# Performance work log

Measured on AMD Instinct MI355X. Metric: run time of the kernel, lower is better.

## Reference

```python
import jax, jax.numpy as jnp
from jax import lax
import numpy as np

RADIUS = 0.1
NSAMPLE = 32
STRIDE = 4
NUM_DIR = 32
BN_EPS = 1e-5


def _fps(p, m):
    # furthest point sampling: p (B,N,3) -> (B,m) int32 indices, start at index 0
    B, N, _ = p.shape

    def step(carry, _):
        dists, last = carry
        lp = jnp.take_along_axis(p, jnp.broadcast_to(last[:, None, None], (B, 1, 3)), axis=1)
        d = jnp.sum((p - lp) ** 2, axis=-1)
        dists = jnp.minimum(dists, d)
        nxt = jnp.argmax(dists, axis=-1).astype(jnp.int32)
        return (dists, nxt), nxt

    last0 = jnp.zeros((B,), jnp.int32)
    d0 = jnp.full((B, N), 1e10, p.dtype)
    _, rest = lax.scan(step, (d0, last0), None, length=m - 1)
    return jnp.concatenate([last0[None, :], rest], axis=0).T  # (B, m)


def _ball_query(q, p, k, radius):
    # q (B,M,3) centers, p (B,N,3) support -> (B,M,k) indices of first k points in ball,
    # padded with the first found index (PointNet++ convention)
    N = p.shape[1]
    d2 = jnp.sum((q[:, :, None, :] - p[:, None, :, :]) ** 2, axis=-1)  # (B,M,N)
    cand = jnp.where(d2 < radius * radius, jnp.arange(N, dtype=jnp.int32), N)
    cand = jnp.sort(cand, axis=-1)[:, :, :k]
    first = cand[:, :, :1]
    return jnp.where(cand == N, first, cand)


def _bn(x, g, b, m, v):
    # BatchNorm1d eval mode on (B,C,N)
    return (x - m[:, None]) * (g[:, None] / jnp.sqrt(v[:, None] + BN_EPS)) + b[:, None]


def _normalize(x, axis):
    return x / jnp.maximum(jnp.linalg.norm(x, axis=axis, keepdims=True), 1e-12)


def setup_inputs() -> dict:
    key = jax.random.key(0)
    ks = jax.random.split(key, 16)
    B, N, Cin, Cout = 4, 8192, 128, 256
    half = Cout // 2
    s = 0.02
    return {
        "p": jax.random.uniform(ks[0], (B, N, 3), jnp.float32),
        "f": jax.random.normal(ks[1], (B, Cin, N), jnp.float32),
        "conv1_w": jax.random.normal(ks[2], (Cout, Cin), jnp.float32) * s,
        "conv1_b": jax.random.normal(ks[3], (Cout,), jnp.float32) * s,
        "skip_w": jax.random.normal(ks[4], (Cout, Cin), jnp.float32) * s,
        "skip_b": jax.random.normal(ks[5], (Cout,), jnp.float32) * s,
        "bn1_g": jnp.ones((Cout,), jnp.float32),
        "bn1_b": jnp.zeros((Cout,), jnp.float32),
        "bn1_m": jax.random.normal(ks[6], (Cout,), jnp.float32) * 0.1,
        "bn1_v": jax.random.uniform(ks[7], (Cout,), jnp.float32) + 0.5,
        "dir_vectors": jax.random.normal(ks[8], (NUM_DIR, 3), jnp.float32),
        "de_w1": jax.random.normal(ks[9], (half, NUM_DIR), jnp.float32) * s,
        "de_g": jnp.ones((half,), jnp.float32),
        "de_bb": jnp.zeros((half,), jnp.float32),
        "de_m": jax.random.normal(ks[10], (half,), jnp.float32) * 0.1,
        "de_v": jax.random.uniform(ks[11], (half,), jnp.float32) + 0.5,
        "de_w2": jax.random.normal(ks[12], (Cout, half), jnp.float32) * s,
        "de_b2": jax.random.normal(ks[13], (Cout,), jnp.float32) * s,
    }


def reference(p, f, conv1_w, conv1_b, skip_w, skip_b, bn1_g, bn1_b, bn1_m, bn1_v,
              dir_vectors, de_w1, de_g, de_bb, de_m, de_v, de_w2, de_b2):
    B, N, _ = p.shape
    Cout = conv1_w.shape[0]
    M, K = N // STRIDE, NSAMPLE

    # FPS sampling + centroid gather
    idx = _fps(p, M)  # (B,M)
    new_p = jnp.take_along_axis(p, jnp.broadcast_to(idx[:, :, None], (B, M, 3)), axis=1)

    # residual branch: gather input feats at centroids, 1x1 conv (bn_after=False)
    fi = jnp.take_along_axis(f, jnp.broadcast_to(idx[:, None, :], (B, f.shape[1], M)), axis=2)
    identity = jnp.einsum('oc,bcm->bom', skip_w, fi) + skip_b[:, None]

    # convs1: 1x1 conv on all N points
    f1 = jnp.einsum('oc,bcn->bon', conv1_w, f) + conv1_b[:, None]  # (B,Cout,N)

    # ball-query grouping
    qidx = _ball_query(new_p, p, K, RADIUS)  # (B,M,K)
    idxf = qidx.reshape(B, M * K)
    gp = jnp.take_along_axis(p, jnp.broadcast_to(idxf[:, :, None], (B, M * K, 3)), axis=1).reshape(B, M, K, 3)
    dp = jnp.transpose(gp - new_p[:, :, None, :], (0, 3, 1, 2))  # (B,3,M,K)
    fj = jnp.take_along_axis(f1, jnp.broadcast_to(idxf[:, None, :], (B, Cout, M * K)), axis=2).reshape(B, Cout, M, K)

    # directional encoding
    dpn = _normalize(dp, axis=1)
    vec = _normalize(dir_vectors, axis=1)  # (NUM_DIR,3)
    theta = jnp.einsum('md,bdnk->bmnk', vec, dpn)  # (B,NUM_DIR,M,K)
    tmax = theta.max(axis=-1)  # (B,NUM_DIR,M)
    h = jnp.einsum('om,bmn->bon', de_w1, tmax)
    h = jax.nn.gelu(_bn(h, de_g, de_bb, de_m, de_v), approximate=False)
    pe = jnp.einsum('oc,bcn->bon', de_w2, h) + de_b2[:, None]

    # neighbor max-pool + BN + residuals
    f_out = _bn(fj.max(axis=-1), bn1_g, bn1_b, bn1_m, bn1_v) + pe + identity
    return new_p, f_out
```

## Files before the change

### kernel.cpp

```cpp
#include <hip/hip_runtime.h>

#define BATCH 4
#define NPTS 8192
#define MPTS 2048
#define CIN 128
#define CO 256
#define KS 32
#define ND 32
#define HALF 128

typedef unsigned int u32;
typedef unsigned long long u64;

#define DPPC_QUAD_XOR1 0xB1
#define DPPC_QUAD_XOR2 0x4E
#define DPPC_ROW_MIRROR 0x140
#define DPPC_ROW_HALF_MIRROR 0x141
#define DPPC_ROW_BCAST15 0x142
#define DPPC_ROW_BCAST31 0x143

template<int CTRL>
__device__ __forceinline__ float dpp_max(float v) {
    int o = __builtin_amdgcn_update_dpp(__float_as_int(-1e30f), __float_as_int(v),
                                        CTRL, 0xF, 0xF, false);
    return fmaxf(v, __int_as_float(o));
}
__device__ __forceinline__ float wave_max_f32(float v) {
    v = dpp_max<DPPC_QUAD_XOR1>(v);
    v = dpp_max<DPPC_QUAD_XOR2>(v);
    v = dpp_max<DPPC_ROW_HALF_MIRROR>(v);
    v = dpp_max<DPPC_ROW_MIRROR>(v);
    v = dpp_max<DPPC_ROW_BCAST15>(v);
    v = dpp_max<DPPC_ROW_BCAST31>(v);
    return __int_as_float(__builtin_amdgcn_readlane(__float_as_int(v), 63));
}

__global__ __launch_bounds__(512) void k_fps(const float* __restrict__ p,
                                             float* __restrict__ out_newp,
                                             int* __restrict__ idx) {
    __shared__ u64 wkey[2][8];
    int b = blockIdx.x, t = threadIdx.x;
    int lane = t & 63, wid = t >> 6;
    const float* pb = p + (size_t)b * NPTS * 3;
    float x[16], y[16], z[16], dist[16];
    int j0 = t * 16;
#pragma unroll
    for (int i = 0; i < 16; ++i) {
        x[i] = pb[(j0 + i) * 3 + 0];
        y[i] = pb[(j0 + i) * 3 + 1];
        z[i] = pb[(j0 + i) * 3 + 2];
        dist[i] = 1e10f;
    }
    float lx = pb[0], ly = pb[1], lz = pb[2];
    if (t == 0) {
        out_newp[(size_t)b * MPTS * 3 + 0] = lx;
        out_newp[(size_t)b * MPTS * 3 + 1] = ly;
        out_newp[(size_t)b * MPTS * 3 + 2] = lz;
        idx[b * MPTS] = 0;
    }
    for (int s = 1; s < MPTS; ++s) {
        int par = s & 1;
        float bv = -1e30f; int bi = 0;
#pragma unroll
        for (int i = 0; i < 16; ++i) {
            float dx = __fsub_rn(x[i], lx);
            float dy = __fsub_rn(y[i], ly);
            float dz = __fsub_rn(z[i], lz);
            float d  = __fadd_rn(__fadd_rn(__fmul_rn(dx, dx), __fmul_rn(dy, dy)),
                                 __fmul_rn(dz, dz));
            float nd = fminf(dist[i], d);
            dist[i] = nd;
            bool gt = nd > bv;
            bi = gt ? i : bi;
            bv = fmaxf(bv, nd);
        }
        float gmw = wave_max_f32(bv);
        u64 mask = __ballot(bv == gmw);
        int first = __ffsll((long long)mask) - 1;
        if (lane == first) {
            int cand = j0 + bi;
            wkey[par][wid] = ((u64)__float_as_uint(gmw) << 32)
                           | (u64)(u32)(NPTS - 1 - cand);
        }
        __syncthreads();
        u64 bestk = wkey[par][0];
#pragma unroll
        for (int ww = 1; ww < 8; ++ww) {
            u64 kk = wkey[par][ww];
            if (kk > bestk) bestk = kk;
        }
        int w0 = (NPTS - 1 - (int)(bestk & 0xFFFFFFFFull)) & (NPTS - 1);
        lx = pb[w0 * 3 + 0]; ly = pb[w0 * 3 + 1]; lz = pb[w0 * 3 + 2];
        if (t == 0) {
            idx[b * MPTS + s] = w0;
            out_newp[((size_t)b * MPTS + s) * 3 + 0] = lx;
            out_newp[((size_t)b * MPTS + s) * 3 + 1] = ly;
            out_newp[((size_t)b * MPTS + s) * 3 + 2] = lz;
        }
    }
}

__global__ __launch_bounds__(256) void k_featz(
    const float* __restrict__ p, const float* __restrict__ f,
    const float* __restrict__ conv1_w, const float* __restrict__ conv1_b,
    const float* __restrict__ skip_w,  const float* __restrict__ skip_b,
    const float* __restrict__ bn1_g, const float* __restrict__ bn1_b,
    const float* __restrict__ bn1_m, const float* __restrict__ bn1_v,
    const float* __restrict__ dirv,  const float* __restrict__ de_w1,
    const float* __restrict__ de_g,  const float* __restrict__ de_bb,
    const float* __restrict__ de_m,  const float* __restrict__ de_v,
    const float* __restrict__ de_w2, const float* __restrict__ de_b2,
    const int* __restrict__ idx,     float* __restrict__ out_f) {
    __shared__ __align__(16) float fg[KS * CIN];
    __shared__ float sdx[KS], sdy[KS], sdz[KS];
    __shared__ float ltm[ND], lfi[CIN], lh[HALF];
    __shared__ int swidx[4][KS];
    __shared__ int scnt[4];
    __shared__ int nb[KS], nbp[KS];

    int q = blockIdx.x;
    int b = q >> 11;
    int m = q & (MPTS - 1);
    int t = threadIdx.x, lane = t & 63, w = t >> 6;
    const float* pb = p + (size_t)b * NPTS * 3;
    int i0 = idx[q] & (NPTS - 1);
    float qx = pb[i0 * 3 + 0], qy = pb[i0 * 3 + 1], qz = pb[i0 * 3 + 2];
    const float R2 = 0.1f * 0.1f;

    int cnt = 0;
    int seg = w * 2048;
    for (int base = 0; base < 2048; base += 64) {
        int j = seg + base + lane;
        float dx = __fsub_rn(pb[j * 3 + 0], qx);
        float dy = __fsub_rn(pb[j * 3 + 1], qy);
        float dz = __fsub_rn(pb[j * 3 + 2], qz);
        float d2 = __fadd_rn(__fadd_rn(__fmul_rn(dx, dx), __fmul_rn(dy, dy)),
                             __fmul_rn(dz, dz));
        bool hit = d2 < R2;
        u64 mask = __ballot(hit);
        if (hit) {
            int pos = cnt + __popcll(mask & ((1ull << lane) - 1ull));
            if (pos < KS) swidx[w][pos] = j;
        }
        cnt += __popcll(mask);
        if (cnt >= KS) break;
    }
    if (lane == 0) scnt[w] = cnt < KS ? cnt : KS;
    __syncthreads();
    int c0s = scnt[0], c1s = scnt[1], c2s = scnt[2], c3s = scnt[3];
    int st1 = c0s, st2 = c0s + c1s, st3 = c0s + c1s + c2s;
    int total = c0s + c1s + c2s + c3s; if (total > KS) total = KS;
    if (total < 1) total = 1;
    if (t < 128) {
        int ww = t >> 5, l = t & 31;
        int stw = (ww == 0) ? 0 : (ww == 1) ? st1 : (ww == 2) ? st2 : st3;
        int cw  = (ww == 0) ? c0s : (ww == 1) ? c1s : (ww == 2) ? c2s : c3s;
        int gp = stw + l;
        if (l < cw && gp < KS) nb[gp] = swidx[ww][l];
    }
    __syncthreads();
    if (t < KS) {
        int jk = nb[t < total ? t : 0] & (NPTS - 1);
        nbp[t] = jk;
        float dx = pb[jk * 3 + 0] - qx;
        float dy = pb[jk * 3 + 1] - qy;
        float dz = pb[jk * 3 + 2] - qz;
        float nr = fmaxf(sqrtf(dx * dx + dy * dy + dz * dz), 1e-12f);
        sdx[t] = dx / nr; sdy[t] = dy / nr; sdz[t] = dz / nr;
    }
    if (t >= 128) {
        lfi[t - 128] = f[((size_t)b * CIN + (t - 128)) * NPTS + i0];
    }
    __syncthreads();
    if (t < ND) {
        float ax = dirv[t * 3], ay = dirv[t * 3 + 1], az = dirv[t * 3 + 2];
        float n = fmaxf(sqrtf(ax * ax + ay * ay + az * az), 1e-12f);
        float vx = ax / n, vy = ay / n, vz = az / n;
        float tm = -1e30f;
#pragma unroll
        for (int k = 0; k < KS; ++k)
            tm = fmaxf(tm, vx * sdx[k] + vy * sdy[k] + vz * sdz[k]);
        ltm[t] = tm;
    }
    for (int e = t; e < KS * CIN; e += 256) {
        int k = e >> 7, i = e & 127;
        fg[k * CIN + i] = f[((size_t)b * CIN + i) * NPTS + nbp[k]];
    }
    __syncthreads();

    int c = t;
    float acc[KS];
#pragma unroll
    for (int k = 0; k < KS; ++k) acc[k] = 0.0f;
    const float4* w4 = (const float4*)(conv1_w + (size_t)c * CIN);
    const float4* fg4 = (const float4*)fg;
    for (int i4 = 0; i4 < 32; ++i4) {
        float4 wv = w4[i4];
#pragma unroll 8
        for (int k = 0; k < KS; ++k) {
            float4 g = fg4[k * 32 + i4];
            acc[k] = fmaf(wv.x, g.x, fmaf(wv.y, g.y,
                     fmaf(wv.z, g.z, fmaf(wv.w, g.w, acc[k]))));
        }
    }
    float bias = conv1_b[c];
    float mx = -1e30f;
#pragma unroll
    for (int k = 0; k < KS; ++k) mx = fmaxf(mx, acc[k] + bias);
    float sc1 = bn1_g[c] / sqrtf(bn1_v[c] + 1e-5f);
    float o1 = (mx - bn1_m[c]) * sc1 + bn1_b[c];

    float idv = skip_b[c];
    {
        const float4* sr = (const float4*)(skip_w + (size_t)c * CIN);
#pragma unroll 8
        for (int r = 0; r < 32; ++r) {
            float4 v = sr[r];
            idv = fmaf(v.x, lfi[r*4+0], fmaf(v.y, lfi[r*4+1],
                  fmaf(v.z, lfi[r*4+2], fmaf(v.w, lfi[r*4+3], idv))));
        }
    }

    {
        int hc = c & (HALF - 1);
        const float4* d1 = (const float4*)(de_w1 + (size_t)hc * ND);
        float a = 0.0f;
#pragma unroll
        for (int r = 0; r < 8; ++r) {
            float4 v = d1[r];
            a = fmaf(v.x, ltm[r*4+0], fmaf(v.y, ltm[r*4+1],
                fmaf(v.z, ltm[r*4+2], fmaf(v.w, ltm[r*4+3], a))));
        }
        float dsc = de_g[hc] / sqrtf(de_v[hc] + 1e-5f);
        float xb = (a - de_m[hc]) * dsc + de_bb[hc];
        float hv = 0.5f * xb * (1.0f + erff(xb * 0.70710678118654752440f));
        if (c < HALF) lh[c] = hv;
    }
    __syncthreads();
    float pe = de_b2[c];
    {
        const float4* d2p = (const float4*)(de_w2 + (size_t)c * HALF);
#pragma unroll 8
        for (int r = 0; r < 32; ++r) {
            float4 v = d2p[r];
            pe = fmaf(v.x, lh[r*4+0], fmaf(v.y, lh[r*4+1],
                 fmaf(v.z, lh[r*4+2], fmaf(v.w, lh[r*4+3], pe))));
        }
    }
    out_f[((size_t)b * CO + c) * MPTS + m] = o1 + pe + idv;
}

extern "C" void kernel_launch(void* const* d_in, const int* in_sizes, int n_in,
                              void* d_out, int out_size, void* d_ws, size_t ws_size,
                              hipStream_t stream) {
    const float* p       = (const float*)d_in[0];
    const float* f       = (const float*)d_in[1];
    const float* conv1_w = (const float*)d_in[2];
    const float* conv1_b = (const float*)d_in[3];
    const float* skip_w  = (const float*)d_in[4];
    const float* skip_b  = (const float*)d_in[5];
    const float* bn1_g   = (const float*)d_in[6];
    const float* bn1_b   = (const float*)d_in[7];
    const float* bn1_m   = (const float*)d_in[8];
    const float* bn1_v   = (const float*)d_in[9];
    const float* dirv    = (const float*)d_in[10];
    const float* de_w1   = (const float*)d_in[11];
    const float* de_g    = (const float*)d_in[12];
    const float* de_bb   = (const float*)d_in[13];
    const float* de_m    = (const float*)d_in[14];
    const float* de_v    = (const float*)d_in[15];
    const float* de_w2   = (const float*)d_in[16];
    const float* de_b2   = (const float*)d_in[17];

    float* out_newp = (float*)d_out;
    float* out_f    = (float*)d_out + (size_t)BATCH * MPTS * 3;
    int*   idx      = (int*)d_ws;

    k_fps  <<<dim3(BATCH),        dim3(512), 0, stream>>>(p, out_newp, idx);
    k_featz<<<dim3(BATCH * MPTS), dim3(256), 0, stream>>>(
        p, f, conv1_w, conv1_b, skip_w, skip_b, bn1_g, bn1_b, bn1_m, bn1_v,
        dirv, de_w1, de_g, de_bb, de_m, de_v, de_w2, de_b2, idx, out_f);
}
```

Measured before the change: 3.091 ms.

## Precompute conv1 over all points and simplify FPS winner lookup

The conv1 1x1 convolution moves out of the per-centroid kernel. A new kernel computes it once for all N points into a transposed workspace buffer, and the feature kernel gathers and max-pools neighbour rows from it instead of recomputing 32x128x256 FMAs per centroid. The FPS kernel now passes the winning point's coordinates through shared memory rather than reloading them from global memory, and stages outputs in LDS with a single write at the end. The new path needs a large workspace and falls back to a per-batch or fully fused path when the workspace is too small.

```diff
diff --git a/kernel.cpp b/kernel.cpp
--- a/kernel.cpp
+++ b/kernel.cpp
@@ -39,6 +39,9 @@
                                              float* __restrict__ out_newp,
                                              int* __restrict__ idx) {
     __shared__ u64 wkey[2][8];
+    __shared__ float wcx[2][8], wcy[2][8], wcz[2][8];
+    __shared__ float obuf[MPTS * 3];
+    __shared__ int   oidx[MPTS];
     int b = blockIdx.x, t = threadIdx.x;
     int lane = t & 63, wid = t >> 6;
     const float* pb = p + (size_t)b * NPTS * 3;
@@ -51,13 +54,12 @@
         z[i] = pb[(j0 + i) * 3 + 2];
         dist[i] = 1e10f;
     }
+#pragma unroll
+    for (int i = 0; i < 16; ++i) {
+        asm volatile("" : "+v"(x[i]), "+v"(y[i]), "+v"(z[i]));
+    }
     float lx = pb[0], ly = pb[1], lz = pb[2];
-    if (t == 0) {
-        out_newp[(size_t)b * MPTS * 3 + 0] = lx;
-        out_newp[(size_t)b * MPTS * 3 + 1] = ly;
-        out_newp[(size_t)b * MPTS * 3 + 2] = lz;
-        idx[b * MPTS] = 0;
-    }
+    if (t == 0) { obuf[0] = lx; obuf[1] = ly; obuf[2] = lz; oidx[0] = 0; }
     for (int s = 1; s < MPTS; ++s) {
         int par = s & 1;
         float bv = -1e30f; int bi = 0;
@@ -78,29 +80,213 @@
         u64 mask = __ballot(bv == gmw);
         int first = __ffsll((long long)mask) - 1;
         if (lane == first) {
-            int cand = j0 + bi;
+            float sx = x[0], sy = y[0], sz = z[0];
+#pragma unroll
+            for (int k = 1; k < 16; ++k) {
+                if (bi == k) { sx = x[k]; sy = y[k]; sz = z[k]; }
+            }
             wkey[par][wid] = ((u64)__float_as_uint(gmw) << 32)
-                           | (u64)(u32)(NPTS - 1 - cand);
+                           | (u64)(u32)(NPTS - 1 - (j0 + bi));
+            wcx[par][wid] = sx; wcy[par][wid] = sy; wcz[par][wid] = sz;
         }
         __syncthreads();
-        u64 bestk = wkey[par][0];
+        u64 bestk = wkey[par][0]; int bw = 0;
 #pragma unroll
         for (int ww = 1; ww < 8; ++ww) {
             u64 kk = wkey[par][ww];
-            if (kk > bestk) bestk = kk;
+            if (kk > bestk) { bestk = kk; bw = ww; }
         }
         int w0 = (NPTS - 1 - (int)(bestk & 0xFFFFFFFFull)) & (NPTS - 1);
-        lx = pb[w0 * 3 + 0]; ly = pb[w0 * 3 + 1]; lz = pb[w0 * 3 + 2];
+        lx = wcx[par][bw]; ly = wcy[par][bw]; lz = wcz[par][bw];
         if (t == 0) {
-            idx[b * MPTS + s] = w0;
-            out_newp[((size_t)b * MPTS + s) * 3 + 0] = lx;
-            out_newp[((size_t)b * MPTS + s) * 3 + 1] = ly;
-            out_newp[((size_t)b * MPTS + s) * 3 + 2] = lz;
-        }
-    }
-}
-
-__global__ __launch_bounds__(256) void k_featz(
+            oidx[s] = w0;
+            obuf[s * 3 + 0] = lx; obuf[s * 3 + 1] = ly; obuf[s * 3 + 2] = lz;
+        }
+    }
+    __syncthreads();
+    for (int e = t; e < MPTS * 3; e += 512) out_newp[(size_t)b * MPTS * 3 + e] = obuf[e];
+    for (int e = t; e < MPTS; e += 512)     idx[b * MPTS + e] = oidx[e];
+}
+
+__global__ __launch_bounds__(256) void k_f1(const float* __restrict__ f,
+                                            const float* __restrict__ conv1_w,
+                                            const float* __restrict__ conv1_b,
+                                            float* __restrict__ f1t, int b0) {
+    __shared__ __align__(16) float fT[CIN * 16];
+    int blk = blockIdx.x;
+    int bl = blk >> 9;
+    int b = b0 + bl;
+    int n0 = (blk & 511) << 4;
+    int t = threadIdx.x;
+    const float* fb = f + (size_t)b * CIN * NPTS;
+    for (int e = t; e < CIN * 16; e += 256) {
+        int k = e >> 4, j = e & 15;
+        fT[e] = fb[(size_t)k * NPTS + n0 + j];
+    }
+    __syncthreads();
+    int c = t;
+    float bias = conv1_b[c];
+    float acc[16];
+#pragma unroll
+    for (int j = 0; j < 16; ++j) acc[j] = bias;
+    const float4* wrow4 = (const float4*)(conv1_w + (size_t)c * CIN);
+    const float4* fT4 = (const float4*)fT;
+    for (int k4 = 0; k4 < 32; ++k4) {
+        float4 wv = wrow4[k4];
+#pragma unroll
+        for (int sub = 0; sub < 4; ++sub) {
+            float w = sub == 0 ? wv.x : sub == 1 ? wv.y : sub == 2 ? wv.z : wv.w;
+            int k = k4 * 4 + sub;
+            float4 a0 = fT4[k*4+0], a1 = fT4[k*4+1], a2 = fT4[k*4+2], a3 = fT4[k*4+3];
+            acc[0]  = fmaf(w, a0.x, acc[0]);  acc[1]  = fmaf(w, a0.y, acc[1]);
+            acc[2]  = fmaf(w, a0.z, acc[2]);  acc[3]  = fmaf(w, a0.w, acc[3]);
+            acc[4]  = fmaf(w, a1.x, acc[4]);  acc[5]  = fmaf(w, a1.y, acc[5]);
+            acc[6]  = fmaf(w, a1.z, acc[6]);  acc[7]  = fmaf(w, a1.w, acc[7]);
+            acc[8]  = fmaf(w, a2.x, acc[8]);  acc[9]  = fmaf(w, a2.y, acc[9]);
+            acc[10] = fmaf(w, a2.z, acc[10]); acc[11] = fmaf(w, a2.w, acc[11]);
+            acc[12] = fmaf(w, a3.x, acc[12]); acc[13] = fmaf(w, a3.y, acc[13]);
+            acc[14] = fmaf(w, a3.z, acc[14]); acc[15] = fmaf(w, a3.w, acc[15]);
+        }
+    }
+    float* dst = f1t + ((size_t)bl * NPTS + n0) * CO + c;
+#pragma unroll
+    for (int j = 0; j < 16; ++j) dst[(size_t)j * CO] = acc[j];
+}
+
+__global__ __launch_bounds__(256) void k_feat(
+    const float* __restrict__ p, const float* __restrict__ f,
+    const float* __restrict__ f1t,
+    const float* __restrict__ skip_w,  const float* __restrict__ skip_b,
+    const float* __restrict__ bn1_g, const float* __restrict__ bn1_b,
+    const float* __restrict__ bn1_m, const float* __restrict__ bn1_v,
+    const float* __restrict__ dirv,  const float* __restrict__ de_w1,
+    const float* __restrict__ de_g,  const float* __restrict__ de_bb,
+    const float* __restrict__ de_m,  const float* __restrict__ de_v,
+    const float* __restrict__ de_w2, const float* __restrict__ de_b2,
+    const int* __restrict__ idx,     float* __restrict__ out_f, int b0) {
+    __shared__ float sdx[KS], sdy[KS], sdz[KS];
+    __shared__ float ltm[ND], lfi[CIN], lh[HALF];
+    __shared__ int swidx[4][KS];
+    __shared__ int scnt[4];
+    __shared__ int nb[KS], nbp[KS];
+
+    int q = b0 * MPTS + blockIdx.x;
+    int b = q >> 11;
+    int bl = b - b0;
+    int m = q & (MPTS - 1);
+    int t = threadIdx.x, lane = t & 63, w = t >> 6;
+    const float* pb = p + (size_t)b * NPTS * 3;
+    int i0 = idx[q] & (NPTS - 1);
+    float qx = pb[i0 * 3 + 0], qy = pb[i0 * 3 + 1], qz = pb[i0 * 3 + 2];
+    const float R2 = 0.1f * 0.1f;
+
+    int cnt = 0;
+    int seg = w * 2048;
+    for (int base = 0; base < 2048; base += 64) {
+        int j = seg + base + lane;
+        float dx = __fsub_rn(pb[j * 3 + 0], qx);
+        float dy = __fsub_rn(pb[j * 3 + 1], qy);
+        float dz = __fsub_rn(pb[j * 3 + 2], qz);
+        float d2 = __fadd_rn(__fadd_rn(__fmul_rn(dx, dx), __fmul_rn(dy, dy)),
+                             __fmul_rn(dz, dz));
+        bool hit = d2 < R2;
+        u64 mask = __ballot(hit);
+        if (hit) {
+            int pos = cnt + __popcll(mask & ((1ull << lane) - 1ull));
+            if (pos < KS) swidx[w][pos] = j;
+        }
+        cnt += __popcll(mask);
+        if (cnt >= KS) break;
+    }
+    if (lane == 0) scnt[w] = cnt < KS ? cnt : KS;
+    __syncthreads();
+    int c0s = scnt[0], c1s = scnt[1], c2s = scnt[2], c3s = scnt[3];
+    int st1 = c0s, st2 = c0s + c1s, st3 = c0s + c1s + c2s;
+    int total = c0s + c1s + c2s + c3s; if (total > KS) total = KS;
+    if (total < 1) total = 1;
+    if (t < 128) {
+        int ww = t >> 5, l = t & 31;
+        int stw = (ww == 0) ? 0 : (ww == 1) ? st1 : (ww == 2) ? st2 : st3;
+        int cw  = (ww == 0) ? c0s : (ww == 1) ? c1s : (ww == 2) ? c2s : c3s;
+        int gp = stw + l;
+        if (l < cw && gp < KS) nb[gp] = swidx[ww][l];
+    }
+    __syncthreads();
+    if (t < KS) {
+        int jk = nb[t < total ? t : 0] & (NPTS - 1);
+        nbp[t] = jk;
+        float dx = pb[jk * 3 + 0] - qx;
+        float dy = pb[jk * 3 + 1] - qy;
+        float dz = pb[jk * 3 + 2] - qz;
+        float nr = fmaxf(sqrtf(dx * dx + dy * dy + dz * dz), 1e-12f);
+        sdx[t] = dx / nr; sdy[t] = dy / nr; sdz[t] = dz / nr;
+    }
+    if (t >= 128) {
+        lfi[t - 128] = f[((size_t)b * CIN + (t - 128)) * NPTS + i0];
+    }
+    __syncthreads();
+    if (t < ND) {
+        float ax = dirv[t * 3], ay = dirv[t * 3 + 1], az = dirv[t * 3 + 2];
+        float n = fmaxf(sqrtf(ax * ax + ay * ay + az * az), 1e-12f);
+        float vx = ax / n, vy = ay / n, vz = az / n;
+        float tm = -1e30f;
+#pragma unroll
+        for (int k = 0; k < KS; ++k)
+            tm = fmaxf(tm, vx * sdx[k] + vy * sdy[k] + vz * sdz[k]);
+        ltm[t] = tm;
+    }
+    __syncthreads();
+
+    int c = t;
+    const float* f1b = f1t + (size_t)bl * NPTS * CO + c;
+    float mx = -1e30f;
+#pragma unroll 8
+    for (int k = 0; k < KS; ++k) {
+        mx = fmaxf(mx, f1b[(size_t)nbp[k] * CO]);
+    }
+    float sc1 = bn1_g[c] / sqrtf(bn1_v[c] + 1e-5f);
+    float o1 = (mx - bn1_m[c]) * sc1 + bn1_b[c];
+
+    float idv = skip_b[c];
+    {
+        const float4* sr = (const float4*)(skip_w + (size_t)c * CIN);
+#pragma unroll 8
+        for (int r = 0; r < 32; ++r) {
+            float4 v = sr[r];
+            idv = fmaf(v.x, lfi[r*4+0], fmaf(v.y, lfi[r*4+1],
+                  fmaf(v.z, lfi[r*4+2], fmaf(v.w, lfi[r*4+3], idv))));
+        }
+    }
+    {
+        int hc = c & (HALF - 1);
+        const float4* d1 = (const float4*)(de_w1 + (size_t)hc * ND);
+        float a = 0.0f;
+#pragma unroll
+        for (int r = 0; r < 8; ++r) {
+            float4 v = d1[r];
+            a = fmaf(v.x, ltm[r*4+0], fmaf(v.y, ltm[r*4+1],
+                fmaf(v.z, ltm[r*4+2], fmaf(v.w, ltm[r*4+3], a))));
+        }
+        float dsc = de_g[hc] / sqrtf(de_v[hc] + 1e-5f);
+        float xb = (a - de_m[hc]) * dsc + de_bb[hc];
+        float hv = 0.5f * xb * (1.0f + erff(xb * 0.70710678118654752440f));
+        if (c < HALF) lh[c] = hv;
+    }
+    __syncthreads();
+    float pe = de_b2[c];
+    {
+        const float4* d2p = (const float4*)(de_w2 + (size_t)c * HALF);
+#pragma unroll 8
+        for (int r = 0; r < 32; ++r) {
+            float4 v = d2p[r];
+            pe = fmaf(v.x, lh[r*4+0], fmaf(v.y, lh[r*4+1],
+                 fmaf(v.z, lh[r*4+2], fmaf(v.w, lh[r*4+3], pe))));
+        }
+    }
+    out_f[((size_t)b * CO + c) * MPTS + m] = o1 + pe + idv;
+}
+
+__global__ __launch_bounds__(256) void k_featz_fused(
     const float* __restrict__ p, const float* __restrict__ f,
     const float* __restrict__ conv1_w, const float* __restrict__ conv1_b,
     const float* __restrict__ skip_w,  const float* __restrict__ skip_b,
@@ -126,7 +312,6 @@
     int i0 = idx[q] & (NPTS - 1);
     float qx = pb[i0 * 3 + 0], qy = pb[i0 * 3 + 1], qz = pb[i0 * 3 + 2];
     const float R2 = 0.1f * 0.1f;
-
     int cnt = 0;
     int seg = w * 2048;
     for (int base = 0; base < 2048; base += 64) {
@@ -168,9 +353,7 @@
         float nr = fmaxf(sqrtf(dx * dx + dy * dy + dz * dz), 1e-12f);
         sdx[t] = dx / nr; sdy[t] = dy / nr; sdz[t] = dz / nr;
     }
-    if (t >= 128) {
-        lfi[t - 128] = f[((size_t)b * CIN + (t - 128)) * NPTS + i0];
-    }
+    if (t >= 128) lfi[t - 128] = f[((size_t)b * CIN + (t - 128)) * NPTS + i0];
     __syncthreads();
     if (t < ND) {
         float ax = dirv[t * 3], ay = dirv[t * 3 + 1], az = dirv[t * 3 + 2];
@@ -187,7 +370,6 @@
         fg[k * CIN + i] = f[((size_t)b * CIN + i) * NPTS + nbp[k]];
     }
     __syncthreads();
-
     int c = t;
     float acc[KS];
 #pragma unroll
@@ -209,7 +391,6 @@
     for (int k = 0; k < KS; ++k) mx = fmaxf(mx, acc[k] + bias);
     float sc1 = bn1_g[c] / sqrtf(bn1_v[c] + 1e-5f);
     float o1 = (mx - bn1_m[c]) * sc1 + bn1_b[c];
-
     float idv = skip_b[c];
     {
         const float4* sr = (const float4*)(skip_w + (size_t)c * CIN);
@@ -220,7 +401,6 @@
                   fmaf(v.z, lfi[r*4+2], fmaf(v.w, lfi[r*4+3], idv))));
         }
     }
-
     {
         int hc = c & (HALF - 1);
         const float4* d1 = (const float4*)(de_w1 + (size_t)hc * ND);
@@ -275,9 +455,30 @@
     float* out_newp = (float*)d_out;
     float* out_f    = (float*)d_out + (size_t)BATCH * MPTS * 3;
     int*   idx      = (int*)d_ws;
-
-    k_fps  <<<dim3(BATCH),        dim3(512), 0, stream>>>(p, out_newp, idx);
-    k_featz<<<dim3(BATCH * MPTS), dim3(256), 0, stream>>>(
-        p, f, conv1_w, conv1_b, skip_w, skip_b, bn1_g, bn1_b, bn1_m, bn1_v,
-        dirv, de_w1, de_g, de_bb, de_m, de_v, de_w2, de_b2, idx, out_f);
-}
+    float* f1t      = (float*)((char*)d_ws + 32768);
+
+    size_t f1_one  = (size_t)NPTS * CO * 4;
+    size_t need_full = 32768 + 4 * f1_one;
+    size_t need_one  = 32768 + f1_one;
+    int mode = (ws_size >= need_full) ? 2 : (ws_size >= need_one) ? 1 : 0;
+
+    k_fps<<<dim3(BATCH), dim3(512), 0, stream>>>(p, out_newp, idx);
+
+    if (mode == 2) {
+        k_f1  <<<dim3(4 * 512),  dim3(256), 0, stream>>>(f, conv1_w, conv1_b, f1t, 0);
+        k_feat<<<dim3(4 * MPTS), dim3(256), 0, stream>>>(
+            p, f, f1t, skip_w, skip_b, bn1_g, bn1_b, bn1_m, bn1_v,
+            dirv, de_w1, de_g, de_bb, de_m, de_v, de_w2, de_b2, idx, out_f, 0);
+    } else if (mode == 1) {
+        for (int b0 = 0; b0 < BATCH; ++b0) {
+            k_f1  <<<dim3(512),  dim3(256), 0, stream>>>(f, conv1_w, conv1_b, f1t, b0);
+            k_feat<<<dim3(MPTS), dim3(256), 0, stream>>>(
+                p, f, f1t, skip_w, skip_b, bn1_g, bn1_b, bn1_m, bn1_v,
+                dirv, de_w1, de_g, de_bb, de_m, de_v, de_w2, de_b2, idx, out_f, b0);
+        }
+    } else {
+        k_featz_fused<<<dim3(BATCH * MPTS), dim3(256), 0, stream>>>(
+            p, f, conv1_w, conv1_b, skip_w, skip_b, bn1_g, bn1_b, bn1_m, bn1_v,
+            dirv, de_w1, de_g, de_bb, de_m, de_v, de_w2, de_b2, idx, out_f);
+    }
+}
```

Result: slower. 3.911 ms (+26.5%).
